# Performance work log

Hardware: AMD Instinct MI355X
Metric: run time of the kernel (lower is better)

The kernel has to match this reference:

```python
import jax, jax.numpy as jnp
import numpy as np

B, N, H, W = 128, 8192, 7, 7


def setup_inputs() -> dict:
    key = jax.random.key(0)
    ks = jax.random.split(key, 10)
    inp = {
        'x': jax.random.normal(ks[0], (B, N, H, W), dtype=jnp.float32),
        'y': jax.random.normal(ks[1], (B, N), dtype=jnp.float32),
        # nn.MultiheadAttention(embed_dim=1, num_heads=1) params (all scalar)
        'wq': jax.random.normal(ks[2], (), dtype=jnp.float32),
        'wk': jax.random.normal(ks[3], (), dtype=jnp.float32),
        'wv': jax.random.normal(ks[4], (), dtype=jnp.float32),
        'bq': jax.random.normal(ks[5], (), dtype=jnp.float32) * 0.1,
        'bk': jax.random.normal(ks[6], (), dtype=jnp.float32) * 0.1,
        'bv': jax.random.normal(ks[7], (), dtype=jnp.float32) * 0.1,
        'wo': jax.random.normal(ks[8], (), dtype=jnp.float32),
        'bo': jax.random.normal(ks[9], (), dtype=jnp.float32) * 0.1,
    }
    return inp


def _mha1(q_src, kv_src, wq, bq, wk, bk, wv, bv, wo, bo):
    # embed_dim=1, num_heads=1, scale = 1/sqrt(1) = 1.
    # torch sees (seq=B, batch=N, embed=1): attention mixes the B axis per n.
    q = q_src * wq + bq            # [B, N]
    k = kv_src * wk + bk           # [B, N]
    v = kv_src * wv + bv           # [B, N]
    scores = jnp.einsum('in,jn->ijn', q, k)      # [B, B, N]
    a = jax.nn.softmax(scores, axis=1)           # softmax over keys j
    out = jnp.einsum('ijn,jn->in', a, v)         # [B, N]
    return out * wo + bo


def reference(x, y, wq, bq, wk, bk, wv, bv, wo, bo):
    xp = jnp.mean(x, axis=(2, 3))                # AdaptiveAvgPool2d((1,1)) -> [B, N]
    self_x = _mha1(xp, xp, wq, bq, wk, bk, wv, bv, wo, bo)
    self_y = _mha1(y, y, wq, bq, wk, bk, wv, bv, wo, bo)
    cross_x = _mha1(xp, y, wq, bq, wk, bk, wv, bv, wo, bo)
    cross_y = _mha1(y, xp, wq, bq, wk, bk, wv, bv, wo, bo)
    f_x = xp + self_x
    f_y = y + self_y
    c_f_x = cross_x + f_x
    c_f_y = cross_y + f_y
    return jnp.concatenate((c_f_x, c_f_y), axis=1)   # [B, 2N]
```

## Files before the change

kernel.cpp:

```cpp
#include <hip/hip_runtime.h>


constexpr int B_SEQ = 128;
constexpr int N_COL = 8192;
constexpr int HWP   = 49;
constexpr int TC    = 8;
constexpr int RG    = 16;
constexpr int NT    = 256;

__global__ __launch_bounds__(NT, 3) void rsca_fused(
    const float* __restrict__ x, const float* __restrict__ y,
    const float* __restrict__ pwq, const float* __restrict__ pwk,
    const float* __restrict__ pwv, const float* __restrict__ pbq,
    const float* __restrict__ pbk, const float* __restrict__ pbv,
    const float* __restrict__ pwo, const float* __restrict__ pbo,
    float* __restrict__ out)
{
    __shared__ float2 kvx[B_SEQ][TC];
    __shared__ float2 kvy[B_SEQ][TC];
    __shared__ float  xstage[RG * TC * HWP];
    __shared__ float  klmn[2][TC], klmx[2][TC];

    const int t  = threadIdx.x;
    const int n0 = blockIdx.x * TC;

    const float wq = pwq[0], wk = pwk[0], wv = pwv[0];
    const float bq = pbq[0], bk = pbk[0], bv = pbv[0];
    const float wo = pwo[0], bo = pbo[0];
    const float L2E = 1.4426950408889634f;
    const float wkL = wk * L2E, bkL = bk * L2E;
    const float alpha = wo * wv;
    const float beta2 = 2.0f * (wo * bv + bo);

    for (int cell = t; cell < B_SEQ * TC; cell += NT) {
        const int b = cell >> 3, c = cell & 7;
        const float yv = y[b * N_COL + n0 + c];
        kvy[b][c] = make_float2(fmaf(yv, wkL, bkL), yv);
    }

    constexpr int ROWF4 = TC * HWP / 4;
    for (int g = 0; g < B_SEQ / RG; ++g) {
        __syncthreads();
        const int b0 = g * RG;
        for (int idx4 = t; idx4 < RG * ROWF4; idx4 += NT) {
            const int bl = idx4 / ROWF4;
            const int r4 = idx4 - bl * ROWF4;
            const float4* src = (const float4*)(x + ((size_t)(b0 + bl) * N_COL + n0) * HWP);
            ((float4*)xstage)[idx4] = src[r4];
        }
        __syncthreads();
        if (t < RG * TC) {
            const int bl = t >> 3, c = t & 7;
            const float* p = xstage + (bl * TC + c) * HWP;
            float s = 0.0f;
            #pragma unroll
            for (int k = 0; k < HWP; ++k) s += p[k];
            const float mean = s * (1.0f / HWP);
            kvx[b0 + bl][c] = make_float2(fmaf(mean, wkL, bkL), mean);
        }
    }
    __syncthreads();

    if (t < 2 * TC) {
        const int c = t & 7, which = t >> 3;
        float mn = 3.4e38f, mx = -3.4e38f;
        for (int j = 0; j < B_SEQ; ++j) {
            const float v = which ? kvy[j][c].x : kvx[j][c].x;
            mn = fminf(mn, v);
            mx = fmaxf(mx, v);
        }
        klmn[which][c] = mn;
        klmx[which][c] = mx;
    }
    __syncthreads();

    const int i  = t & (B_SEQ - 1);
    const int ch = t >> 7;
    #pragma unroll
    for (int cc = 0; cc < TC / 2; ++cc) {
        const int c = ch + 2 * cc;
        const float xi = kvx[i][c].y;
        const float yi = kvy[i][c].y;
        const float qx = fmaf(xi, wq, bq);
        const float qy = fmaf(yi, wq, bq);
        const float msx = qx >= 0.0f ? qx * klmx[0][c] : qx * klmn[0][c];
        const float mcy = qy >= 0.0f ? qy * klmx[0][c] : qy * klmn[0][c];
        const float msy = qy >= 0.0f ? qy * klmx[1][c] : qy * klmn[1][c];
        const float mcx = qx >= 0.0f ? qx * klmx[1][c] : qx * klmn[1][c];

        float s0sx = 0.f, s1sx = 0.f, s0cy = 0.f, s1cy = 0.f;
        float s0sy = 0.f, s1sy = 0.f, s0cx = 0.f, s1cx = 0.f;
        #pragma unroll 4
        for (int j = 0; j < B_SEQ; ++j) {
            const float2 kx = kvx[j][c];
            const float2 ky = kvy[j][c];
            const float e1 = __builtin_amdgcn_exp2f(fmaf(qx, kx.x, -msx));
            const float e2 = __builtin_amdgcn_exp2f(fmaf(qy, kx.x, -mcy));
            const float e3 = __builtin_amdgcn_exp2f(fmaf(qy, ky.x, -msy));
            const float e4 = __builtin_amdgcn_exp2f(fmaf(qx, ky.x, -mcx));
            s1sx = fmaf(e1, kx.y, s1sx); s0sx += e1;
            s1cy = fmaf(e2, kx.y, s1cy); s0cy += e2;
            s1sy = fmaf(e3, ky.y, s1sy); s0sy += e3;
            s1cx = fmaf(e4, ky.y, s1cx); s0cx += e4;
        }
        const float mx_sx = s1sx * __builtin_amdgcn_rcpf(s0sx);
        const float mx_cx = s1cx * __builtin_amdgcn_rcpf(s0cx);
        const float my_sy = s1sy * __builtin_amdgcn_rcpf(s0sy);
        const float my_cy = s1cy * __builtin_amdgcn_rcpf(s0cy);
        const float outx = fmaf(alpha, mx_sx + mx_cx, beta2 + xi);
        const float outy = fmaf(alpha, my_sy + my_cy, beta2 + yi);
        out[(size_t)i * (2 * N_COL) + n0 + c]         = outx;
        out[(size_t)i * (2 * N_COL) + N_COL + n0 + c] = outy;
    }
}

extern "C" void kernel_launch(void* const* d_in, const int* in_sizes, int n_in,
                              void* d_out, int out_size, void* d_ws, size_t ws_size,
                              hipStream_t stream) {
    const float* x   = (const float*)d_in[0];
    const float* y   = (const float*)d_in[1];
    const float* pwq = (const float*)d_in[2];
    const float* pwk = (const float*)d_in[3];
    const float* pwv = (const float*)d_in[4];
    const float* pbq = (const float*)d_in[5];
    const float* pbk = (const float*)d_in[6];
    const float* pbv = (const float*)d_in[7];
    const float* pwo = (const float*)d_in[8];
    const float* pbo = (const float*)d_in[9];
    float* out = (float*)d_out;

    rsca_fused<<<dim3(N_COL / TC), dim3(NT), 0, stream>>>(
        x, y, pwq, pwk, pwv, pbq, pbk, pbv, pwo, pbo, out);
}
```

Baseline: 381.1 us.

## Split pooling into a streaming kernel and run attention on pooled workspace

Splits the fused kernel in two. A grid-stride pooling kernel streams x in contiguous tiles into a workspace of means, and a separate attention kernel reads the pooled values and y. The attention kernel halves its column tile, transposes its shared-memory layout, parallelises the min/max reduction, and register-blocks the key loop by 8. The aim is contiguous, high-bandwidth reads of the dominant x traffic and higher occupancy, at the cost of an extra launch and a workspace round trip.

```diff
diff --git a/kernel.cpp b/kernel.cpp
--- a/kernel.cpp
+++ b/kernel.cpp
@@ -4,21 +4,45 @@
 constexpr int B_SEQ = 128;
 constexpr int N_COL = 8192;
 constexpr int HWP   = 49;
-constexpr int TC    = 8;
-constexpr int RG    = 16;
 constexpr int NT    = 256;
+constexpr int TC    = 4;
+constexpr int PC    = 128;
 
-__global__ __launch_bounds__(NT, 3) void rsca_fused(
-    const float* __restrict__ x, const float* __restrict__ y,
+__global__ __launch_bounds__(NT) void rsca_pool(
+    const float* __restrict__ x, float* __restrict__ xp)
+{
+    __shared__ float st[PC * HWP];
+    const int t = threadIdx.x;
+    const int ntiles = (B_SEQ * N_COL) / PC;
+    for (int tile = blockIdx.x; tile < ntiles; tile += gridDim.x) {
+        const size_t cell0 = (size_t)tile * PC;
+        const float4* src = (const float4*)(x + cell0 * HWP);
+        __syncthreads();
+        for (int k = t; k < PC * HWP / 4; k += NT)
+            ((float4*)st)[k] = src[k];
+        __syncthreads();
+        const int cell = t >> 1, half = t & 1;
+        const float* p = st + cell * HWP + half * 25;
+        float s = 0.0f;
+        #pragma unroll
+        for (int k = 0; k < 24; ++k) s += p[k];
+        if (half == 0) s += p[24];
+        s += __shfl_xor(s, 1);
+        if (half == 0) xp[cell0 + cell] = s * (1.0f / HWP);
+    }
+}
+
+__global__ __launch_bounds__(NT, 6) void rsca_attn(
+    const float* __restrict__ xp, const float* __restrict__ y,
     const float* __restrict__ pwq, const float* __restrict__ pwk,
     const float* __restrict__ pwv, const float* __restrict__ pbq,
     const float* __restrict__ pbk, const float* __restrict__ pbv,
     const float* __restrict__ pwo, const float* __restrict__ pbo,
     float* __restrict__ out)
 {
-    __shared__ float2 kvx[B_SEQ][TC];
-    __shared__ float2 kvy[B_SEQ][TC];
-    __shared__ float  xstage[RG * TC * HWP];
+    __shared__ float2 kvxT[TC][B_SEQ];
+    __shared__ float2 kvyT[TC][B_SEQ];
+    __shared__ float  pmn[2][TC][8], pmx[2][TC][8];
     __shared__ float  klmn[2][TC], klmx[2][TC];
 
     const int t  = threadIdx.x;
@@ -33,84 +57,83 @@
     const float beta2 = 2.0f * (wo * bv + bo);
 
     for (int cell = t; cell < B_SEQ * TC; cell += NT) {
-        const int b = cell >> 3, c = cell & 7;
-        const float yv = y[b * N_COL + n0 + c];
-        kvy[b][c] = make_float2(fmaf(yv, wkL, bkL), yv);
-    }
-
-    constexpr int ROWF4 = TC * HWP / 4;
-    for (int g = 0; g < B_SEQ / RG; ++g) {
-        __syncthreads();
-        const int b0 = g * RG;
-        for (int idx4 = t; idx4 < RG * ROWF4; idx4 += NT) {
-            const int bl = idx4 / ROWF4;
-            const int r4 = idx4 - bl * ROWF4;
-            const float4* src = (const float4*)(x + ((size_t)(b0 + bl) * N_COL + n0) * HWP);
-            ((float4*)xstage)[idx4] = src[r4];
-        }
-        __syncthreads();
-        if (t < RG * TC) {
-            const int bl = t >> 3, c = t & 7;
-            const float* p = xstage + (bl * TC + c) * HWP;
-            float s = 0.0f;
-            #pragma unroll
-            for (int k = 0; k < HWP; ++k) s += p[k];
-            const float mean = s * (1.0f / HWP);
-            kvx[b0 + bl][c] = make_float2(fmaf(mean, wkL, bkL), mean);
-        }
+        const int j = cell >> 2, c = cell & 3;
+        const float fx = xp[(size_t)j * N_COL + n0 + c];
+        const float fy = y [(size_t)j * N_COL + n0 + c];
+        kvxT[c][j] = make_float2(fmaf(fx, wkL, bkL), fx);
+        kvyT[c][j] = make_float2(fmaf(fy, wkL, bkL), fy);
     }
     __syncthreads();
 
-    if (t < 2 * TC) {
-        const int c = t & 7, which = t >> 3;
+    if (t < 64) {
+        const int set = t >> 5, c = (t >> 3) & 3, part = t & 7;
         float mn = 3.4e38f, mx = -3.4e38f;
-        for (int j = 0; j < B_SEQ; ++j) {
-            const float v = which ? kvy[j][c].x : kvx[j][c].x;
+        #pragma unroll
+        for (int k = 0; k < 16; ++k) {
+            const int j = part * 16 + k;
+            const float v = set ? kvyT[c][j].x : kvxT[c][j].x;
             mn = fminf(mn, v);
             mx = fmaxf(mx, v);
         }
-        klmn[which][c] = mn;
-        klmx[which][c] = mx;
+        pmn[set][c][part] = mn;
+        pmx[set][c][part] = mx;
+    }
+    __syncthreads();
+    if (t < 8) {
+        const int set = t >> 2, c = t & 3;
+        float mn = 3.4e38f, mx = -3.4e38f;
+        #pragma unroll
+        for (int k = 0; k < 8; ++k) {
+            mn = fminf(mn, pmn[set][c][k]);
+            mx = fmaxf(mx, pmx[set][c][k]);
+        }
+        klmn[set][c] = mn;
+        klmx[set][c] = mx;
     }
     __syncthreads();
 
     const int i  = t & (B_SEQ - 1);
     const int ch = t >> 7;
     #pragma unroll
-    for (int cc = 0; cc < TC / 2; ++cc) {
-        const int c = ch + 2 * cc;
-        const float xi = kvx[i][c].y;
-        const float yi = kvy[i][c].y;
+    for (int cc = 0; cc < 2; ++cc) {
+        const int c = ch * 2 + cc;
+        const float2* __restrict__ px = kvxT[c];
+        const float2* __restrict__ py = kvyT[c];
+        const float xi = px[i].y;
+        const float yi = py[i].y;
         const float qx = fmaf(xi, wq, bq);
         const float qy = fmaf(yi, wq, bq);
-        const float msx = qx >= 0.0f ? qx * klmx[0][c] : qx * klmn[0][c];
-        const float mcy = qy >= 0.0f ? qy * klmx[0][c] : qy * klmn[0][c];
-        const float msy = qy >= 0.0f ? qy * klmx[1][c] : qy * klmn[1][c];
-        const float mcx = qx >= 0.0f ? qx * klmx[1][c] : qx * klmn[1][c];
+        const float nmsx = -(qx >= 0.0f ? qx * klmx[0][c] : qx * klmn[0][c]);
+        const float nmcy = -(qy >= 0.0f ? qy * klmx[0][c] : qy * klmn[0][c]);
+        const float nmsy = -(qy >= 0.0f ? qy * klmx[1][c] : qy * klmn[1][c]);
+        const float nmcx = -(qx >= 0.0f ? qx * klmx[1][c] : qx * klmn[1][c]);
 
         float s0sx = 0.f, s1sx = 0.f, s0cy = 0.f, s1cy = 0.f;
         float s0sy = 0.f, s1sy = 0.f, s0cx = 0.f, s1cx = 0.f;
-        #pragma unroll 4
-        for (int j = 0; j < B_SEQ; ++j) {
-            const float2 kx = kvx[j][c];
-            const float2 ky = kvy[j][c];
-            const float e1 = __builtin_amdgcn_exp2f(fmaf(qx, kx.x, -msx));
-            const float e2 = __builtin_amdgcn_exp2f(fmaf(qy, kx.x, -mcy));
-            const float e3 = __builtin_amdgcn_exp2f(fmaf(qy, ky.x, -msy));
-            const float e4 = __builtin_amdgcn_exp2f(fmaf(qx, ky.x, -mcx));
-            s1sx = fmaf(e1, kx.y, s1sx); s0sx += e1;
-            s1cy = fmaf(e2, kx.y, s1cy); s0cy += e2;
-            s1sy = fmaf(e3, ky.y, s1sy); s0sy += e3;
-            s1cx = fmaf(e4, ky.y, s1cx); s0cx += e4;
+        for (int j0 = 0; j0 < B_SEQ; j0 += 8) {
+            float2 kx[8], ky[8];
+            #pragma unroll
+            for (int jj = 0; jj < 8; ++jj) kx[jj] = px[j0 + jj];
+            #pragma unroll
+            for (int jj = 0; jj < 8; ++jj) ky[jj] = py[j0 + jj];
+            #pragma unroll
+            for (int jj = 0; jj < 8; ++jj) {
+                const float e1 = __builtin_amdgcn_exp2f(fmaf(qx, kx[jj].x, nmsx));
+                const float e2 = __builtin_amdgcn_exp2f(fmaf(qy, kx[jj].x, nmcy));
+                const float e3 = __builtin_amdgcn_exp2f(fmaf(qy, ky[jj].x, nmsy));
+                const float e4 = __builtin_amdgcn_exp2f(fmaf(qx, ky[jj].x, nmcx));
+                s1sx = fmaf(e1, kx[jj].y, s1sx); s0sx += e1;
+                s1cy = fmaf(e2, kx[jj].y, s1cy); s0cy += e2;
+                s1sy = fmaf(e3, ky[jj].y, s1sy); s0sy += e3;
+                s1cx = fmaf(e4, ky[jj].y, s1cx); s0cx += e4;
+            }
         }
-        const float mx_sx = s1sx * __builtin_amdgcn_rcpf(s0sx);
-        const float mx_cx = s1cx * __builtin_amdgcn_rcpf(s0cx);
-        const float my_sy = s1sy * __builtin_amdgcn_rcpf(s0sy);
-        const float my_cy = s1cy * __builtin_amdgcn_rcpf(s0cy);
-        const float outx = fmaf(alpha, mx_sx + mx_cx, beta2 + xi);
-        const float outy = fmaf(alpha, my_sy + my_cy, beta2 + yi);
-        out[(size_t)i * (2 * N_COL) + n0 + c]         = outx;
-        out[(size_t)i * (2 * N_COL) + N_COL + n0 + c] = outy;
+        const float mx_attn = s1sx * __builtin_amdgcn_rcpf(s0sx)
+                            + s1cx * __builtin_amdgcn_rcpf(s0cx);
+        const float my_attn = s1sy * __builtin_amdgcn_rcpf(s0sy)
+                            + s1cy * __builtin_amdgcn_rcpf(s0cy);
+        out[(size_t)i * (2 * N_COL) + n0 + c]         = fmaf(alpha, mx_attn, beta2 + xi);
+        out[(size_t)i * (2 * N_COL) + N_COL + n0 + c] = fmaf(alpha, my_attn, beta2 + yi);
     }
 }
 
@@ -127,8 +150,10 @@
     const float* pbv = (const float*)d_in[7];
     const float* pwo = (const float*)d_in[8];
     const float* pbo = (const float*)d_in[9];
+    float* xp  = (float*)d_ws;
     float* out = (float*)d_out;
 
-    rsca_fused<<<dim3(N_COL / TC), dim3(NT), 0, stream>>>(
-        x, y, pwq, pwk, pwv, pbq, pbk, pbv, pwo, pbo, out);
+    rsca_pool<<<dim3(2048), dim3(NT), 0, stream>>>(x, xp);
+    rsca_attn<<<dim3(N_COL / TC), dim3(NT), 0, stream>>>(
+        xp, y, pwq, pwk, pwv, pbq, pbk, pbv, pwo, pbo, out);
 }
```

Result: no change. 377.5 us (-0.9%).
